# Performance work log

Measured on AMD Instinct MI355X. Metric: run time of the kernel, lower is better.

The kernel has to match this reference:

```python
import jax, jax.numpy as jnp
import numpy as np

DIM = 1024
HEADS = 16
DIM_HEAD = 64
INNER = HEADS * DIM_HEAD
SCALE = DIM_HEAD ** -0.5


def setup_inputs() -> dict:
    key = jax.random.key(0)
    ks = jax.random.split(key, 9)
    B, N = 4, 4096
    x = jax.random.normal(ks[0], (B, N, DIM), dtype=jnp.float32)
    mask = jnp.ones((B, N), dtype=bool)
    s = 0.02
    W_qkv = jax.random.normal(ks[1], (DIM, INNER * 3), dtype=jnp.float32) * s
    w_q = jax.random.normal(ks[2], (DIM_HEAD,), dtype=jnp.float32) * s
    w_k = jax.random.normal(ks[3], (DIM_HEAD,), dtype=jnp.float32) * s
    W_r = jax.random.normal(ks[4], (DIM_HEAD, DIM_HEAD), dtype=jnp.float32) * s
    b_r = jnp.zeros((DIM_HEAD,), dtype=jnp.float32)
    W_out = jax.random.normal(ks[5], (INNER, DIM), dtype=jnp.float32) * s
    b_out = jnp.zeros((DIM,), dtype=jnp.float32)
    return {"x": x, "mask": mask, "W_qkv": W_qkv, "w_q": w_q, "w_k": w_k,
            "W_r": W_r, "b_r": b_r, "W_out": W_out, "b_out": b_out}


def reference(x, mask, W_qkv, w_q, w_k, W_r, b_r, W_out, b_out):
    B, N, D = x.shape
    h, dh = HEADS, DIM_HEAD
    mask_value = -jnp.finfo(x.dtype).max

    qkv = x @ W_qkv                                  # [B,N,3*inner]
    q, k, v = jnp.split(qkv, 3, axis=-1)
    tohead = lambda t: t.reshape(B, N, h, dh).transpose(0, 2, 1, 3)  # b h n d
    q, k, v = tohead(q), tohead(k), tohead(v)
    m = mask[:, None, :]                             # b 1 n

    # global query via softmax-pooled per-token logits
    q_logits = jnp.einsum('bhnd,d->bhn', q, w_q) * SCALE
    q_attn = jax.nn.softmax(jnp.where(m, q_logits, mask_value), axis=-1)
    global_q = jnp.einsum('bhn,bhnd->bhd', q_attn, q)[:, :, None, :]  # b h 1 d

    k = k * global_q
    k_logits = jnp.einsum('bhnd,d->bhn', k, w_k) * SCALE
    k_attn = jax.nn.softmax(jnp.where(m, k_logits, mask_value), axis=-1)
    global_k = jnp.einsum('bhn,bhnd->bhd', k_attn, k)[:, :, None, :]  # b h 1 d

    v = v * global_k
    r = jnp.einsum('bhnd,de->bhne', v, W_r) + b_r + q  # to_r(v) + q
    r = r.transpose(0, 2, 1, 3).reshape(B, N, h * dh)  # b n (h d)
    return r @ W_out + b_out
```

## Files before the change

kernel.cpp:

```cpp
#include <hip/hip_runtime.h>
#include <hip/hip_bf16.h>
#include <math.h>

#define B_    4
#define N_    4096
#define D_    1024
#define H_    16
#define DH_   64
#define M_TOT (B_ * N_)
#define QKV3  (3 * D_)
#define SCALE_ 0.125f
#define NSPLIT 16

typedef float f32x4 __attribute__((ext_vector_type(4)));
typedef __bf16 bf16x8 __attribute__((ext_vector_type(8)));
typedef unsigned short u16;
typedef unsigned int u32;

__device__ __forceinline__ float bf2f(u16 u) {
    union { u32 i; float f; } v; v.i = ((u32)u) << 16; return v.f;
}
__device__ __forceinline__ u16 f2bf(float f) {
    union { float f; u32 i; } v; v.f = f;
    u32 r = (v.i + 0x7fffu + ((v.i >> 16) & 1u)) >> 16;
    return (u16)r;
}

__global__ __launch_bounds__(256) void prep(const float* __restrict__ x, u16* __restrict__ xb,
                                            const float* __restrict__ Wqkv, u16* __restrict__ wqkv,
                                            const float* __restrict__ Wout, u16* __restrict__ wout) {
    __shared__ float t[32][33];
    const int bid = blockIdx.x, tid = threadIdx.x;
    if (bid < 16384) {
        const int i = bid * 256 + tid;
        float4 v = ((const float4*)x)[i];
        ushort4 o;
        o.x = f2bf(v.x); o.y = f2bf(v.y); o.z = f2bf(v.z); o.w = f2bf(v.w);
        ((ushort4*)xb)[i] = o;
        return;
    }
    const float* in; u16* out; int K, N, bx, by;
    if (bid < 16384 + 3072) {
        const int b2 = bid - 16384;
        in = Wqkv; out = wqkv; K = D_; N = QKV3; bx = b2 % 96; by = b2 / 96;
    } else {
        const int b2 = bid - 19456;
        in = Wout; out = wout; K = D_; N = D_; bx = b2 & 31; by = b2 >> 5;
    }
    const int n0 = bx * 32, k0 = by * 32;
    const int tx = tid & 31, ty = tid >> 5;
#pragma unroll
    for (int r = 0; r < 32; r += 8)
        t[ty + r][tx] = in[(size_t)(k0 + ty + r) * N + n0 + tx];
    __syncthreads();
#pragma unroll
    for (int r = 0; r < 32; r += 8)
        out[(size_t)(n0 + ty + r) * K + k0 + tx] = f2bf(t[tx][ty + r]);
}

#define BM 256
#define BN 256
#define BK 32

template <bool SCATTER, bool SWIZ>
__global__ __launch_bounds__(512, 2) void gemm_bt(const u16* __restrict__ A,
                                                  const u16* __restrict__ Bt,
                                                  void* __restrict__ Cout,
                                                  const float* __restrict__ bias,
                                                  int M, int N, int K) {
    __shared__ u16 lds[65536];
    const int tid = threadIdx.x;
    const int lane = tid & 63, wave = tid >> 6;
    const int wm = wave >> 2, wn = wave & 3;
    u32 bx = blockIdx.x, by = blockIdx.y;
    if (SWIZ) {
        const u32 nwg = gridDim.x * gridDim.y;
        const u32 lid = by * gridDim.x + bx;
        const u32 chunk = nwg >> 3;
        const u32 nid = (lid & 7) * chunk + (lid >> 3);
        bx = nid % gridDim.x; by = nid / gridDim.x;
    }
    const int m0 = by * BM, n0 = bx * BN;

    const int srow = tid >> 2;
    const int scol = 8 * ((tid & 3) ^ ((tid >> 3) & 3));
    const u16* aSrc = A + (size_t)(m0 + srow) * K + scol;
    const u16* bSrc = Bt + (size_t)(n0 + srow) * K + scol;
    const u32 dOff = (u32)wave * 512u;

    const int cbu = 8 * ((lane >> 4) ^ ((lane >> 1) & 3));
    const u32 arow = (u32)(wm * 128 + (lane & 15)) * 32u + cbu;
    const u32 brow = 32768u + (u32)(wn * 64 + (lane & 15)) * 32u + cbu;

    f32x4 acc[8][4] = {};

#define GLOAD(src, off) __builtin_amdgcn_global_load_lds(                          \
        (__attribute__((address_space(1))) const void*)(src),                      \
        (__attribute__((address_space(3))) void*)&lds[off], 16, 0, 0)
#define STAGE(t) { const size_t ko = (size_t)(t) * BK; const u32 sb_ = ((t) & 3) * 8192u; \
        GLOAD(aSrc + ko,                   sb_ + dOff);                            \
        GLOAD(aSrc + ko + (size_t)128 * K, sb_ + 4096u + dOff);                    \
        GLOAD(bSrc + ko,                   32768u + sb_ + dOff);                   \
        GLOAD(bSrc + ko + (size_t)128 * K, 32768u + sb_ + 4096u + dOff); }

    const int NT = K >> 5;
    STAGE(0); STAGE(1); STAGE(2);

    for (int t = 0; t < NT; ++t) {
        if (t + 3 <= NT)      asm volatile("s_waitcnt vmcnt(8)" ::: "memory");
        else if (t + 2 == NT) asm volatile("s_waitcnt vmcnt(4)" ::: "memory");
        else                  asm volatile("s_waitcnt vmcnt(0)" ::: "memory");
        __builtin_amdgcn_s_barrier();
        if (t + 3 < NT) STAGE(t + 3);

        const u32 sb = (u32)(t & 3) * 8192u;
        bf16x8 af[8], bfr[4];
#pragma unroll
        for (int i = 0; i < 8; i++) af[i] = *(const bf16x8*)&lds[sb + arow + i * 512];
#pragma unroll
        for (int j = 0; j < 4; j++) bfr[j] = *(const bf16x8*)&lds[sb + brow + j * 512];
        __builtin_amdgcn_s_setprio(1);
#pragma unroll
        for (int i = 0; i < 8; i++)
#pragma unroll
            for (int j = 0; j < 4; j++)
                acc[i][j] = __builtin_amdgcn_mfma_f32_16x16x32_bf16(af[i], bfr[j], acc[i][j], 0, 0, 0);
        __builtin_amdgcn_s_setprio(0);
    }
#undef STAGE
#undef GLOAD

    __syncthreads();
    const int cr = (lane >> 4) * 4;
    const int cc = lane & 15;
    u16* reg = &lds[(u32)wave * 8192u];

    if (SCATTER) {
#pragma unroll
        for (int i = 0; i < 8; i++)
#pragma unroll
            for (int j = 0; j < 4; j++)
#pragma unroll
                for (int r = 0; r < 4; r++)
                    reg[(i * 16 + cr + r) * 64 + j * 16 + cc] = f2bf(acc[i][j][r]);
        const int colb = n0 + wn * 64;
        const int part = colb >> 10, hh = (colb >> 6) & (H_ - 1);
        const int grow0 = m0 + wm * 128;
        const int bb = grow0 >> 12, nn0 = grow0 & (N_ - 1);
        u16* plane = (u16*)Cout + (((size_t)(part * B_ + bb) * H_ + hh) * N_) * DH_;
        const int lr8 = lane >> 3, le = (lane & 7) * 8;
#pragma unroll
        for (int p = 0; p < 16; p++) {
            const int lr = p * 8 + lr8;
            const uint4 w = *(const uint4*)&reg[lr * 64 + le];
            *(uint4*)(plane + (size_t)(nn0 + lr) * DH_ + le) = w;
        }
    } else {
        float* regf = (float*)reg;
        const int lr4 = lane >> 4, le4 = (lane & 15) * 4;
        float bv[4];
#pragma unroll
        for (int j = 0; j < 4; j++)
            bv[j] = bias ? bias[n0 + wn * 64 + j * 16 + cc] : 0.f;
#pragma unroll
        for (int h = 0; h < 2; h++) {
#pragma unroll
            for (int i2 = 0; i2 < 4; i2++) {
                const int i = h * 4 + i2;
#pragma unroll
                for (int j = 0; j < 4; j++)
#pragma unroll
                    for (int r = 0; r < 4; r++)
                        regf[(i2 * 16 + cr + r) * 64 + j * 16 + cc] = acc[i][j][r] + bv[j];
            }
#pragma unroll
            for (int p = 0; p < 16; p++) {
                const int lr = p * 4 + lr4;
                const float4 w = *(const float4*)&regf[lr * 64 + le4];
                *(float4*)((float*)Cout + (size_t)(m0 + wm * 128 + h * 64 + lr) * N
                           + n0 + wn * 64 + le4) = w;
            }
            if (!h) __syncthreads();
        }
    }
}

template <bool KPHASE>
__global__ __launch_bounds__(256) void pool_partial(const u16* __restrict__ plane,
                                                    const float* __restrict__ wvec,
                                                    const float* __restrict__ partq,
                                                    float* __restrict__ part) {
    __shared__ float sm[32], sl[32], sacc[32][64];
    __shared__ float gqsh[64];
    const int bh = blockIdx.x, s = blockIdx.y;
    const int tid = threadIdx.x;
    const int sub = tid >> 3, j = tid & 7;
    const size_t base = (size_t)bh * N_ * DH_ + (size_t)s * (N_ / NSPLIT) * DH_ + j * 8;

    if (KPHASE) {
        if (tid < 64) {
            float M = -INFINITY;
            for (int t = 0; t < NSPLIT; t++) M = fmaxf(M, partq[((size_t)bh * NSPLIT + t) * 66]);
            float L = 0.f, ssum = 0.f;
            for (int t = 0; t < NSPLIT; t++) {
                const float* o = partq + ((size_t)bh * NSPLIT + t) * 66;
                const float e = __expf(o[0] - M);
                L += o[1] * e;
                ssum += o[2 + tid] * e;
            }
            gqsh[tid] = ssum / L;
        }
        __syncthreads();
    }

    float wv[8], gq[8];
#pragma unroll
    for (int i = 0; i < 8; i++) wv[i] = wvec[j * 8 + i];
    if (KPHASE) {
#pragma unroll
        for (int i = 0; i < 8; i++) gq[i] = gqsh[j * 8 + i];
    }

    float m = -INFINITY, l = 0.f, acc[8];
#pragma unroll
    for (int i = 0; i < 8; i++) acc[i] = 0.f;
    const int ITER = N_ / NSPLIT / 32;
    uint4 raw = *(const uint4*)(plane + base + (size_t)sub * DH_);
    for (int it = 0; it < ITER; it++) {
        uint4 nxt;
        if (it + 1 < ITER)
            nxt = *(const uint4*)(plane + base + (size_t)((it + 1) * 32 + sub) * DH_);
        const u16* pu = (const u16*)&raw;
        float f[8], p = 0.f;
#pragma unroll
        for (int i = 0; i < 8; i++) {
            f[i] = bf2f(pu[i]);
            if (KPHASE) f[i] *= gq[i];
            p += f[i] * wv[i];
        }
        p += __shfl_xor(p, 1); p += __shfl_xor(p, 2); p += __shfl_xor(p, 4);
        p *= SCALE_;
        const float mn = fmaxf(m, p);
        const float sc = __expf(m - mn);
        const float w = __expf(p - mn);
        m = mn; l = l * sc + w;
#pragma unroll
        for (int i = 0; i < 8; i++) acc[i] = acc[i] * sc + w * f[i];
        raw = nxt;
    }
    if (j == 0) { sm[sub] = m; sl[sub] = l; }
#pragma unroll
    for (int i = 0; i < 8; i++) sacc[sub][j * 8 + i] = acc[i];
    __syncthreads();
    if (tid < 64) {
        float M = -INFINITY;
        for (int g = 0; g < 32; g++) M = fmaxf(M, sm[g]);
        float L = 0.f, ssum = 0.f;
        for (int g = 0; g < 32; g++) {
            const float e = __expf(sm[g] - M);
            L += sl[g] * e;
            ssum += sacc[g][tid] * e;
        }
        float* o = part + ((size_t)bh * NSPLIT + s) * 66;
        if (tid == 0) { o[0] = M; o[1] = L; }
        o[2 + tid] = ssum;
    }
}

__global__ __launch_bounds__(256) void apply_r_mfma(const u16* __restrict__ qkv,
                                                    const float* __restrict__ Wr,
                                                    const float* __restrict__ br,
                                                    const float* __restrict__ partk,
                                                    u16* __restrict__ rout) {
    __shared__ u16 Mt[64][136];
    __shared__ float gksh[64];
    __shared__ u16 rb[4][64 * 64];
    const int bh = blockIdx.y;
    const int b = bh >> 4, h = bh & 15;
    const int tid = threadIdx.x, lane = tid & 63, wave = tid >> 6;

    if (tid < 64) {
        float M = -INFINITY;
        for (int t = 0; t < NSPLIT; t++) M = fmaxf(M, partk[((size_t)bh * NSPLIT + t) * 66]);
        float L = 0.f, ssum = 0.f;
        for (int t = 0; t < NSPLIT; t++) {
            const float* o = partk + ((size_t)bh * NSPLIT + t) * 66;
            const float e = __expf(o[0] - M);
            L += o[1] * e;
            ssum += o[2 + tid] * e;
        }
        gksh[tid] = ssum / L;
    }
    __syncthreads();

    for (int idx = tid; idx < 4096; idx += 256) {
        const int d = idx >> 6, e = idx & 63;
        Mt[e][d] = f2bf(gksh[d] * Wr[idx]);
        Mt[e][64 + d] = (d == e) ? (u16)0x3F80 : (u16)0;
    }
    __syncthreads();

    const size_t qbase = (size_t)bh * N_ * DH_;
    const size_t vbase = (size_t)(2 * B_ * H_ + bh) * N_ * DH_;
    const int row0 = blockIdx.x * 256 + wave * 64;
    const int fr = lane & 15;
    const int fk8 = (lane >> 4) * 8;
    f32x4 acc[4][4] = {};

#pragma unroll
    for (int ks = 0; ks < 4; ks++) {
        const int kd = ks * 32 + fk8;
        bf16x8 af[4], bf[4];
#pragma unroll
        for (int i = 0; i < 4; i++) {
            const int row = row0 + i * 16 + fr;
            const size_t off = (kd < 64) ? (vbase + (size_t)row * DH_ + kd)
                                         : (qbase + (size_t)row * DH_ + (kd - 64));
            af[i] = *(const bf16x8*)(qkv + off);
        }
#pragma unroll
        for (int j = 0; j < 4; j++)
            bf[j] = *(const bf16x8*)&Mt[j * 16 + fr][kd];
#pragma unroll
        for (int i = 0; i < 4; i++)
#pragma unroll
            for (int j = 0; j < 4; j++)
                acc[i][j] = __builtin_amdgcn_mfma_f32_16x16x32_bf16(af[i], bf[j], acc[i][j], 0, 0, 0);
    }

    const int cr = (lane >> 4) * 4;
    const int cc = lane & 15;
#pragma unroll
    for (int j = 0; j < 4; j++) {
        const float bv = br[j * 16 + cc];
#pragma unroll
        for (int i = 0; i < 4; i++)
#pragma unroll
            for (int r = 0; r < 4; r++)
                rb[wave][(i * 16 + cr + r) * 64 + j * 16 + cc] = f2bf(acc[i][j][r] + bv);
    }
    const int lr8 = lane >> 3, le = (lane & 7) * 8;
#pragma unroll
    for (int p = 0; p < 8; p++) {
        const int lr = p * 8 + lr8;
        const uint4 w = *(const uint4*)&rb[wave][lr * 64 + le];
        *(uint4*)(rout + (size_t)(b * N_ + row0 + lr) * D_ + h * DH_ + le) = w;
    }
}

extern "C" void kernel_launch(void* const* d_in, const int* in_sizes, int n_in,
                              void* d_out, int out_size, void* d_ws, size_t ws_size,
                              hipStream_t stream) {
    const float* x = (const float*)d_in[0];
    const float* W_qkv = (const float*)d_in[2];
    const float* w_q = (const float*)d_in[3];
    const float* w_k = (const float*)d_in[4];
    const float* W_r = (const float*)d_in[5];
    const float* b_r = (const float*)d_in[6];
    const float* W_out = (const float*)d_in[7];
    const float* b_out = (const float*)d_in[8];
    float* out = (float*)d_out;

    u16* xb = (u16*)d_ws;
    u16* wqkv = xb + (size_t)M_TOT * D_;
    u16* wout = wqkv + (size_t)QKV3 * D_;
    u16* qkv = wout + (size_t)D_ * D_;
    u16* rbuf = qkv + (size_t)M_TOT * QKV3;
    float* partq = (float*)(rbuf + (size_t)M_TOT * D_);
    float* partk = partq + 64 * NSPLIT * 66;

    prep<<<16384 + 3072 + 1024, 256, 0, stream>>>(x, xb, W_qkv, wqkv, W_out, wout);

    gemm_bt<true, true><<<dim3(QKV3 / BN, M_TOT / BM), 512, 0, stream>>>(
        xb, wqkv, qkv, nullptr, M_TOT, QKV3, D_);

    pool_partial<false><<<dim3(64, NSPLIT), 256, 0, stream>>>(qkv, w_q, nullptr, partq);
    pool_partial<true><<<dim3(64, NSPLIT), 256, 0, stream>>>(
        qkv + (size_t)(B_ * H_) * N_ * DH_, w_k, partq, partk);

    apply_r_mfma<<<dim3(N_ / 256, 64), 256, 0, stream>>>(qkv, W_r, b_r, partk, rbuf);

    gemm_bt<false, true><<<dim3(D_ / BN, M_TOT / BM), 512, 0, stream>>>(
        rbuf, wout, out, b_out, M_TOT, D_, D_);
}
```

Before: 331.9 us.

## Double GEMM K-tile to 64 with two-stage buffering, coarsen prep, halve pool splits

Raises the GEMM K-tile from 32 to 64 and swaps the four-deep, three-ahead prefetch pipeline for a two-buffer scheme with a full vmcnt(0) wait each iteration. The LDS swizzle changes to an 8-way XOR to match. The intent is fewer barriers per K and more MFMA work per sync, at the cost of less latency hiding. It also makes each prep block convert 8 float4s instead of one (fewer blocks) and halves NSPLIT in the pooling kernels.

```diff
diff --git a/kernel.cpp b/kernel.cpp
--- a/kernel.cpp
+++ b/kernel.cpp
@@ -10,7 +10,7 @@
 #define M_TOT (B_ * N_)
 #define QKV3  (3 * D_)
 #define SCALE_ 0.125f
-#define NSPLIT 16
+#define NSPLIT 8
 
 typedef float f32x4 __attribute__((ext_vector_type(4)));
 typedef __bf16 bf16x8 __attribute__((ext_vector_type(8)));
@@ -31,20 +31,24 @@
                                             const float* __restrict__ Wout, u16* __restrict__ wout) {
     __shared__ float t[32][33];
     const int bid = blockIdx.x, tid = threadIdx.x;
-    if (bid < 16384) {
-        const int i = bid * 256 + tid;
-        float4 v = ((const float4*)x)[i];
-        ushort4 o;
-        o.x = f2bf(v.x); o.y = f2bf(v.y); o.z = f2bf(v.z); o.w = f2bf(v.w);
-        ((ushort4*)xb)[i] = o;
+    if (bid < 2048) {
+        const int base = bid * 2048 + tid;
+#pragma unroll
+        for (int k = 0; k < 8; k++) {
+            const int i = base + k * 256;
+            float4 v = ((const float4*)x)[i];
+            ushort4 o;
+            o.x = f2bf(v.x); o.y = f2bf(v.y); o.z = f2bf(v.z); o.w = f2bf(v.w);
+            ((ushort4*)xb)[i] = o;
+        }
         return;
     }
     const float* in; u16* out; int K, N, bx, by;
-    if (bid < 16384 + 3072) {
-        const int b2 = bid - 16384;
+    if (bid < 2048 + 3072) {
+        const int b2 = bid - 2048;
         in = Wqkv; out = wqkv; K = D_; N = QKV3; bx = b2 % 96; by = b2 / 96;
     } else {
-        const int b2 = bid - 19456;
+        const int b2 = bid - 5120;
         in = Wout; out = wout; K = D_; N = D_; bx = b2 & 31; by = b2 >> 5;
     }
     const int n0 = bx * 32, k0 = by * 32;
@@ -60,7 +64,7 @@
 
 #define BM 256
 #define BN 256
-#define BK 32
+#define BK 64
 
 template <bool SCATTER, bool SWIZ>
 __global__ __launch_bounds__(512, 2) void gemm_bt(const u16* __restrict__ A,
@@ -82,49 +86,52 @@
     }
     const int m0 = by * BM, n0 = bx * BN;
 
-    const int srow = tid >> 2;
-    const int scol = 8 * ((tid & 3) ^ ((tid >> 3) & 3));
+    const int srow = tid >> 3;
+    const int scol = 8 * ((tid & 7) ^ (srow & 7));
     const u16* aSrc = A + (size_t)(m0 + srow) * K + scol;
     const u16* bSrc = Bt + (size_t)(n0 + srow) * K + scol;
     const u32 dOff = (u32)wave * 512u;
 
-    const int cbu = 8 * ((lane >> 4) ^ ((lane >> 1) & 3));
-    const u32 arow = (u32)(wm * 128 + (lane & 15)) * 32u + cbu;
-    const u32 brow = 32768u + (u32)(wn * 64 + (lane & 15)) * 32u + cbu;
+    const u32 cbu0 = 8u * (u32)(((lane >> 4)    ) ^ (lane & 7));
+    const u32 cbu1 = 8u * (u32)(((lane >> 4) + 4) ^ (lane & 7));
+    const u32 arow = (u32)(wm * 128 + (lane & 15)) * 64u;
+    const u32 brow = 32768u + (u32)(wn * 64 + (lane & 15)) * 64u;
 
     f32x4 acc[8][4] = {};
 
 #define GLOAD(src, off) __builtin_amdgcn_global_load_lds(                          \
         (__attribute__((address_space(1))) const void*)(src),                      \
         (__attribute__((address_space(3))) void*)&lds[off], 16, 0, 0)
-#define STAGE(t) { const size_t ko = (size_t)(t) * BK; const u32 sb_ = ((t) & 3) * 8192u; \
-        GLOAD(aSrc + ko,                   sb_ + dOff);                            \
-        GLOAD(aSrc + ko + (size_t)128 * K, sb_ + 4096u + dOff);                    \
-        GLOAD(bSrc + ko,                   32768u + sb_ + dOff);                   \
-        GLOAD(bSrc + ko + (size_t)128 * K, 32768u + sb_ + 4096u + dOff); }
-
-    const int NT = K >> 5;
-    STAGE(0); STAGE(1); STAGE(2);
+#define STAGE(t) { const size_t ko = (size_t)(t) * BK; const u32 sb_ = ((t) & 1) * 16384u; \
+        _Pragma("unroll") for (int p = 0; p < 4; p++)                              \
+            GLOAD(aSrc + ko + (size_t)(p * 64) * K, sb_ + p * 4096u + dOff);       \
+        _Pragma("unroll") for (int p = 0; p < 4; p++)                              \
+            GLOAD(bSrc + ko + (size_t)(p * 64) * K, 32768u + sb_ + p * 4096u + dOff); }
+
+    const int NT = K >> 6;
+    STAGE(0);
 
     for (int t = 0; t < NT; ++t) {
-        if (t + 3 <= NT)      asm volatile("s_waitcnt vmcnt(8)" ::: "memory");
-        else if (t + 2 == NT) asm volatile("s_waitcnt vmcnt(4)" ::: "memory");
-        else                  asm volatile("s_waitcnt vmcnt(0)" ::: "memory");
+        asm volatile("s_waitcnt vmcnt(0)" ::: "memory");
         __builtin_amdgcn_s_barrier();
-        if (t + 3 < NT) STAGE(t + 3);
-
-        const u32 sb = (u32)(t & 3) * 8192u;
-        bf16x8 af[8], bfr[4];
-#pragma unroll
-        for (int i = 0; i < 8; i++) af[i] = *(const bf16x8*)&lds[sb + arow + i * 512];
-#pragma unroll
-        for (int j = 0; j < 4; j++) bfr[j] = *(const bf16x8*)&lds[sb + brow + j * 512];
+        if (t + 1 < NT) STAGE(t + 1);
+
+        const u32 sb = (u32)(t & 1) * 16384u;
         __builtin_amdgcn_s_setprio(1);
 #pragma unroll
-        for (int i = 0; i < 8; i++)
-#pragma unroll
-            for (int j = 0; j < 4; j++)
-                acc[i][j] = __builtin_amdgcn_mfma_f32_16x16x32_bf16(af[i], bfr[j], acc[i][j], 0, 0, 0);
+        for (int kc = 0; kc < 2; kc++) {
+            const u32 cb = kc ? cbu1 : cbu0;
+            bf16x8 af[8], bfr[4];
+#pragma unroll
+            for (int i = 0; i < 8; i++) af[i] = *(const bf16x8*)&lds[sb + arow + i * 1024 + cb];
+#pragma unroll
+            for (int j = 0; j < 4; j++) bfr[j] = *(const bf16x8*)&lds[sb + brow + j * 1024 + cb];
+#pragma unroll
+            for (int i = 0; i < 8; i++)
+#pragma unroll
+                for (int j = 0; j < 4; j++)
+                    acc[i][j] = __builtin_amdgcn_mfma_f32_16x16x32_bf16(af[i], bfr[j], acc[i][j], 0, 0, 0);
+        }
         __builtin_amdgcn_s_setprio(0);
     }
 #undef STAGE
@@ -369,7 +376,7 @@
     float* partq = (float*)(rbuf + (size_t)M_TOT * D_);
     float* partk = partq + 64 * NSPLIT * 66;
 
-    prep<<<16384 + 3072 + 1024, 256, 0, stream>>>(x, xb, W_qkv, wqkv, W_out, wout);
+    prep<<<6144, 256, 0, stream>>>(x, xb, W_qkv, wqkv, W_out, wout);
 
     gemm_bt<true, true><<<dim3(QKV3 / BN, M_TOT / BM), 512, 0, stream>>>(
         xb, wqkv, qkv, nullptr, M_TOT, QKV3, D_);
```

Measured after the change: 327.4 us. About the same (-1.4%).
